# Performance work log

Hardware: AMD Instinct MI355X
Metric: run time of the kernel (lower is better)

The kernel has to match this reference:

```python
import jax, jax.numpy as jnp
import numpy as np

B, C, INTER, H, W = 4, 256, 128, 64, 64
EPS = 1e-5

def conv1x1(x, w, b):
    # x: [B,Cin,H,W], w: [Cout,Cin], b: [Cout]
    return jnp.einsum('bchw,oc->bohw', x, w) + b[None, :, None, None]

def setup_inputs() -> dict:
    key = jax.random.key(0)
    ks = jax.random.split(key, 12)
    sc_in = 1.0 / np.sqrt(C)
    sc_int = 1.0 / np.sqrt(INTER)
    return {
        'x': jax.random.normal(ks[0], (B, C, H, W), dtype=jnp.float32),
        'g_w': jax.random.normal(ks[1], (INTER, C), dtype=jnp.float32) * sc_in,
        'g_b': jax.random.normal(ks[2], (INTER,), dtype=jnp.float32) * 0.01,
        'theta_w': jax.random.normal(ks[3], (INTER, C), dtype=jnp.float32) * sc_in,
        'theta_b': jax.random.normal(ks[4], (INTER,), dtype=jnp.float32) * 0.01,
        'phi_w': jax.random.normal(ks[5], (INTER, C), dtype=jnp.float32) * sc_in,
        'phi_b': jax.random.normal(ks[6], (INTER,), dtype=jnp.float32) * 0.01,
        'w_w': jax.random.normal(ks[7], (C, INTER), dtype=jnp.float32) * sc_int,
        'w_b': jax.random.normal(ks[8], (C,), dtype=jnp.float32) * 0.01,
        'gamma': jax.random.normal(ks[9], (C,), dtype=jnp.float32) * 0.1 + 1.0,
        'beta': jax.random.normal(ks[10], (C,), dtype=jnp.float32) * 0.1,
    }

def reference(x, g_w, g_b, theta_w, theta_b, phi_w, phi_b, w_w, w_b, gamma, beta):
    b, c, h, w = x.shape
    n = h * w
    g_x = conv1x1(x, g_w, g_b).reshape(b, INTER, n).transpose(0, 2, 1)      # [b,n,d]
    theta_x = conv1x1(x, theta_w, theta_b).reshape(b, INTER, n).transpose(0, 2, 1)  # [b,n,d]
    phi_x = conv1x1(x, phi_w, phi_b).reshape(b, INTER, n)                   # [b,d,n]
    f = jnp.einsum('bnd,bdm->bnm', theta_x, phi_x)                          # [b,n,n]
    f_div_c = jax.nn.softmax(f, axis=-1)
    y = jnp.einsum('bnm,bmd->bnd', f_div_c, g_x)                            # [b,n,d]
    y = y.transpose(0, 2, 1).reshape(b, INTER, h, w)                        # [b,d,h,w]
    w_y = conv1x1(y, w_w, w_b)                                              # [b,c,h,w]
    # BatchNorm2d (training mode: batch statistics, biased variance)
    mean = jnp.mean(w_y, axis=(0, 2, 3), keepdims=True)
    var = jnp.var(w_y, axis=(0, 2, 3), keepdims=True)
    bn = (w_y - mean) * jax.lax.rsqrt(var + EPS)
    bn = bn * gamma[None, :, None, None] + beta[None, :, None, None]
    return bn + x
```

## Files before the change

### kernel.cpp

```cpp
#include <hip/hip_runtime.h>

#define B_ 4
#define C_ 256
#define D_ 128
#define N_ 4096
#define BN_ 16384

typedef unsigned short u16t;
typedef _Float16 f16t;
typedef f16t f16x8 __attribute__((ext_vector_type(8)));
typedef f16t f16x4 __attribute__((ext_vector_type(4)));
typedef float f32x4 __attribute__((ext_vector_type(4)));

static __device__ __forceinline__ u16t f2h(float f) {
  f16t h = (f16t)f; u16t u; __builtin_memcpy(&u, &h, 2); return u;
}
static __device__ __forceinline__ float h2f(u16t u) {
  f16t h; __builtin_memcpy(&h, &u, 2); return (float)h;
}

static __device__ __forceinline__ void gld_lds16(const u16t* g, u16t* l) {
  __builtin_amdgcn_global_load_lds(
      (const __attribute__((address_space(1))) void*)g,
      (__attribute__((address_space(3))) void*)l, 16, 0, 0);
}

__global__ __launch_bounds__(256) void prep_w(const float* __restrict__ th_w,
                                              const float* __restrict__ ph_w,
                                              const float* __restrict__ th_b,
                                              const float* __restrict__ ph_b,
                                              const float* __restrict__ g_w,
                                              const float* __restrict__ w_w,
                                              u16t* __restrict__ Wc, u16t* __restrict__ gwc,
                                              u16t* __restrict__ wwc, float* __restrict__ bc) {
  const int idx = blockIdx.x * 256 + threadIdx.x;
  if (idx < 65536) {
    const int j = idx >> 8, c = idx & 255;
    const float v = (j < 128) ? th_w[j * 256 + c] : ph_w[(j - 128) * 256 + c];
    Wc[idx] = f2h(v);
  } else if (idx < 98304) {
    const int i = idx - 65536;
    gwc[i] = f2h(g_w[i]);
  } else if (idx < 131072) {
    const int i = idx - 98304;
    wwc[i] = f2h(w_w[i]);
  } else if (idx < 131328) {
    const int j = idx - 131072;
    bc[j] = (j < 128) ? th_b[j] : ph_b[j - 128];
  }
}

__global__ __launch_bounds__(256) void transpose_x(const float* __restrict__ x,
                                                   u16t* __restrict__ xT) {
  __shared__ u16t t[32][33];
  const int b = blockIdx.z, c0 = blockIdx.y * 32, n0 = blockIdx.x * 32;
  const int tid = threadIdx.x;
  {
    const int cl = tid >> 3, n4 = (tid & 7) * 4;
    const float4 v = *(const float4*)(x + ((size_t)b * C_ + c0 + cl) * N_ + n0 + n4);
    t[n4 + 0][cl] = f2h(v.x);
    t[n4 + 1][cl] = f2h(v.y);
    t[n4 + 2][cl] = f2h(v.z);
    t[n4 + 3][cl] = f2h(v.w);
  }
  __syncthreads();
  {
    const int nl = tid >> 3, c4 = (tid & 7) * 4;
    unsigned int lo = (unsigned int)t[nl][c4 + 0] | ((unsigned int)t[nl][c4 + 1] << 16);
    unsigned int hi = (unsigned int)t[nl][c4 + 2] | ((unsigned int)t[nl][c4 + 3] << 16);
    uint2 o; o.x = lo; o.y = hi;
    *(uint2*)(xT + ((size_t)b * N_ + n0 + nl) * C_ + c0 + c4) = o;
  }
}

__global__ __launch_bounds__(256)
void gemm_qkv(const u16t* __restrict__ xT, const u16t* __restrict__ Wc,
              const u16t* __restrict__ gwc, const float* __restrict__ bc,
              const float* __restrict__ g_b, u16t* __restrict__ QKo,
              u16t* __restrict__ Vo) {
  __shared__ __attribute__((aligned(16))) u16t lA[128 * 40];
  __shared__ __attribute__((aligned(16))) u16t lB[128 * 40];
  const int z = blockIdx.z, bx = blockIdx.x;
  const u16t* xTb = xT + (size_t)z * N_ * C_;
  const u16t* A; const u16t* B; u16t* Cb; int ldc, m0, j0, colb;
  const float* bias;
  if (bx < 64) {
    A = xTb; B = Wc; Cb = QKo + (size_t)z * N_ * 256; ldc = 256;
    m0 = (bx >> 1) * 128; j0 = (bx & 1) * 128; bias = bc; colb = 1;
  } else {
    A = gwc; B = xTb; Cb = Vo + (size_t)z * D_ * N_; ldc = N_;
    m0 = 0; j0 = (bx - 64) * 128; bias = g_b; colb = 0;
  }
  const int tid = threadIdx.x, lane = tid & 63, wave = tid >> 6;
  const int quad = lane >> 4, l16 = lane & 15;
  const int wm = wave & 1, wj = wave >> 1;

  const f32x4 zero = {0.f, 0.f, 0.f, 0.f};
  f32x4 acc[4][4];
#pragma unroll
  for (int mi = 0; mi < 4; ++mi)
#pragma unroll
    for (int ji = 0; ji < 4; ++ji) acc[mi][ji] = zero;

  for (int k0 = 0; k0 < 256; k0 += 32) {
#pragma unroll
    for (int rr = 0; rr < 2; ++rr) {
      const int idx = rr * 256 + tid;
      const int row = idx >> 2, sg = idx & 3;
      *(uint4*)&lA[row * 40 + sg * 8] = *(const uint4*)(A + (size_t)(m0 + row) * 256 + k0 + sg * 8);
      *(uint4*)&lB[row * 40 + sg * 8] = *(const uint4*)(B + (size_t)(j0 + row) * 256 + k0 + sg * 8);
    }
    __syncthreads();
    f16x8 af[4], bfr[4];
#pragma unroll
    for (int i = 0; i < 4; ++i)
      af[i] = *(const f16x8*)&lA[(wm * 64 + i * 16 + l16) * 40 + quad * 8];
#pragma unroll
    for (int i = 0; i < 4; ++i)
      bfr[i] = *(const f16x8*)&lB[(wj * 64 + i * 16 + l16) * 40 + quad * 8];
#pragma unroll
    for (int mi = 0; mi < 4; ++mi)
#pragma unroll
      for (int ji = 0; ji < 4; ++ji)
        acc[mi][ji] = __builtin_amdgcn_mfma_f32_16x16x32_f16(af[mi], bfr[ji], acc[mi][ji], 0, 0, 0);
    __syncthreads();
  }

  float cb[4];
  if (colb) {
#pragma unroll
    for (int ji = 0; ji < 4; ++ji) cb[ji] = bias[j0 + wj * 64 + ji * 16 + l16];
  }
#pragma unroll
  for (int mi = 0; mi < 4; ++mi) {
#pragma unroll
    for (int r = 0; r < 4; ++r) {
      const int row = m0 + wm * 64 + mi * 16 + quad * 4 + r;
      const float rb = colb ? 0.f : bias[row];
#pragma unroll
      for (int ji = 0; ji < 4; ++ji) {
        const int col = j0 + wj * 64 + ji * 16 + l16;
        const float v = acc[mi][ji][r] + (colb ? cb[ji] : rb);
        Cb[(size_t)row * ldc + col] = f2h(v);
      }
    }
  }
}

__global__ __launch_bounds__(256, 2)
void attn(const u16t* __restrict__ QK, const u16t* __restrict__ V,
          u16t* __restrict__ On0, u16t* __restrict__ On1, float* __restrict__ ml) {
  const int b = blockIdx.y;
  const int split = blockIdx.z;
  const int n0 = blockIdx.x * 128;
  const int kv0 = split * (N_ / 4);
  const int tid = threadIdx.x, lane = tid & 63, wave = tid >> 6;
  const int quad = lane >> 4, l16 = lane & 15;
  const int x7 = l16 & 7;
  __shared__ __attribute__((aligned(16))) u16t Ks[2][64 * 128];
  __shared__ __attribute__((aligned(16))) u16t Vs[2][128 * 64];
  const u16t* QKb = QK + (size_t)b * N_ * 256;
  const u16t* Vb  = V  + (size_t)b * D_ * N_;

  const int krow_l = lane >> 4, kchunk_l = lane & 15;
  const int vrow_l = lane >> 3, vchunk_l = lane & 7;

  f16x8 qf[2][4];
#pragma unroll
  for (int qi = 0; qi < 2; ++qi) {
    const u16t* qrow = QKb + (size_t)(n0 + wave * 32 + qi * 16 + l16) * 256;
#pragma unroll
    for (int kc = 0; kc < 4; ++kc)
      qf[qi][kc] = *(const f16x8*)(qrow + kc * 32 + quad * 8);
  }

  const f32x4 zero = {0.f, 0.f, 0.f, 0.f};
  f32x4 o[2][8];
#pragma unroll
  for (int qi = 0; qi < 2; ++qi)
#pragma unroll
    for (int db = 0; db < 8; ++db) o[qi][db] = zero;
  float m[2] = {-1e30f, -1e30f}, l[2] = {0.f, 0.f};

#pragma unroll
  for (int i = 0; i < 4; ++i) {
    const int krow = (wave * 4 + i) * 4 + krow_l;
    const int kcl = kchunk_l ^ (krow & 7);
    gld_lds16(QKb + (size_t)(kv0 + krow) * 256 + 128 + kcl * 8,
              &Ks[0][(wave * 4 + i) * 512]);
  }
#pragma unroll
  for (int i = 0; i < 4; ++i) {
    const int vrow = (wave * 4 + i) * 8 + vrow_l;
    const int vcl = vchunk_l ^ (vrow & 7);
    gld_lds16(Vb + (size_t)vrow * N_ + kv0 + vcl * 8,
              &Vs[0][(wave * 4 + i) * 512]);
  }
  __syncthreads();

  int cur = 0;
  for (int it = 0; it < 16; ++it) {
    if (it < 15) {
      const int kvn = kv0 + (it + 1) * 64;
#pragma unroll
      for (int i = 0; i < 4; ++i) {
        const int krow = (wave * 4 + i) * 4 + krow_l;
        const int kcl = kchunk_l ^ (krow & 7);
        gld_lds16(QKb + (size_t)(kvn + krow) * 256 + 128 + kcl * 8,
                  &Ks[cur ^ 1][(wave * 4 + i) * 512]);
      }
#pragma unroll
      for (int i = 0; i < 4; ++i) {
        const int vrow = (wave * 4 + i) * 8 + vrow_l;
        const int vcl = vchunk_l ^ (vrow & 7);
        gld_lds16(Vb + (size_t)vrow * N_ + kvn + vcl * 8,
                  &Vs[cur ^ 1][(wave * 4 + i) * 512]);
      }
    }

    const u16t* KsC = &Ks[cur][0];
    const u16t* VsC = &Vs[cur][0];

    f32x4 s[2][4];
#pragma unroll
    for (int qi = 0; qi < 2; ++qi)
#pragma unroll
      for (int ci = 0; ci < 4; ++ci) s[qi][ci] = zero;
#pragma unroll
    for (int kc = 0; kc < 4; ++kc) {
#pragma unroll
      for (int ci = 0; ci < 4; ++ci) {
        f16x8 kf = *(const f16x8*)&KsC[(ci * 16 + l16) * 128 + (((kc * 4 + quad) ^ x7) << 3)];
        s[0][ci] = __builtin_amdgcn_mfma_f32_16x16x32_f16(kf, qf[0][kc], s[0][ci], 0, 0, 0);
        s[1][ci] = __builtin_amdgcn_mfma_f32_16x16x32_f16(kf, qf[1][kc], s[1][ci], 0, 0, 0);
      }
    }

    float al[2];
    f16x4 pb[2][4];
#pragma unroll
    for (int qi = 0; qi < 2; ++qi) {
      float mx = s[qi][0][0];
#pragma unroll
      for (int ci = 0; ci < 4; ++ci)
#pragma unroll
        for (int r = 0; r < 4; ++r) mx = fmaxf(mx, s[qi][ci][r]);
      mx = fmaxf(mx, __shfl_xor(mx, 16));
      mx = fmaxf(mx, __shfl_xor(mx, 32));
      const float mnew = fmaxf(m[qi], mx);
      al[qi] = __expf(m[qi] - mnew);
      float psum = 0.f;
#pragma unroll
      for (int ci = 0; ci < 4; ++ci) {
#pragma unroll
        for (int r = 0; r < 4; ++r) {
          const float p = __expf(s[qi][ci][r] - mnew);
          psum += p;
          pb[qi][ci][r] = (f16t)p;
        }
      }
      psum += __shfl_xor(psum, 16);
      psum += __shfl_xor(psum, 32);
      l[qi] = l[qi] * al[qi] + psum;
      m[qi] = mnew;
    }

#pragma unroll
    for (int qi = 0; qi < 2; ++qi)
#pragma unroll
      for (int db = 0; db < 8; ++db) {
#pragma unroll
        for (int r = 0; r < 4; ++r) o[qi][db][r] *= al[qi];
      }
#pragma unroll
    for (int ci = 0; ci < 4; ++ci) {
#pragma unroll
      for (int db = 0; db < 8; ++db) {
        f16x4 av = *(const f16x4*)&VsC[(db * 16 + l16) * 64 +
                                       (((ci * 2 + (quad >> 1)) ^ x7) << 3) + (quad & 1) * 4];
        o[0][db] = __builtin_amdgcn_mfma_f32_16x16x16f16(av, pb[0][ci], o[0][db], 0, 0, 0);
        o[1][db] = __builtin_amdgcn_mfma_f32_16x16x16f16(av, pb[1][ci], o[1][db], 0, 0, 0);
      }
    }
    __syncthreads();
    cur ^= 1;
  }

  u16t* Onb = (split < 2) ? On0 : On1;
  const int sp = split & 1;
#pragma unroll
  for (int qi = 0; qi < 2; ++qi) {
    const int q = n0 + wave * 32 + qi * 16 + l16;
    const float inv = 1.0f / l[qi];
    u16t* yrow = Onb + (((size_t)sp * B_ + b) * N_ + q) * D_;
#pragma unroll
    for (int db = 0; db < 8; ++db) {
      f16x4 pk;
#pragma unroll
      for (int r = 0; r < 4; ++r) pk[r] = (f16t)(o[qi][db][r] * inv);
      *(f16x4*)(yrow + db * 16 + quad * 4) = pk;
    }
    if (quad == 0) {
      float* mlp = ml + ((size_t)split * BN_ + (size_t)b * N_ + q) * 2;
      mlp[0] = m[qi]; mlp[1] = l[qi];
    }
  }
}

__global__ __launch_bounds__(256)
void gemm_wy(const u16t* __restrict__ wwc, const u16t* __restrict__ O0,
             const u16t* __restrict__ O2, const float* __restrict__ ml,
             u16t* __restrict__ wy, const float* __restrict__ w_b) {
  __shared__ __attribute__((aligned(16))) u16t lA[4][128 * 40];
  __shared__ __attribute__((aligned(16))) u16t lB[4][64 * 40];
  __shared__ float wrow[64][4];
  const int z = blockIdx.z;
  const int m0 = blockIdx.y * 128, j0 = blockIdx.x * 64;
  const int tid = threadIdx.x, lane = tid & 63, wave = tid >> 6;
  const int quad = lane >> 4, l16 = lane & 15;
  const int wm = wave & 1, wj = wave >> 1;
  const size_t halfO = (size_t)BN_ * D_;

  uint4 b0[4], b1[4], b2[4], b3[4];
#pragma unroll
  for (int cs = 0; cs < 4; ++cs) {
    const int cid = cs * 256 + tid;
    const int row = cid >> 4, sg = cid & 15;
    const size_t base = ((size_t)z * N_ + j0 + row) * D_ + sg * 8;
    b0[cs] = *(const uint4*)(O0 + base);
    b1[cs] = *(const uint4*)(O0 + halfO + base);
    b2[cs] = *(const uint4*)(O2 + base);
    b3[cs] = *(const uint4*)(O2 + halfO + base);
  }
  uint4 aw[8];
#pragma unroll
  for (int as = 0; as < 8; ++as) {
    const int cid = as * 256 + tid;
    const int row = cid >> 4, sg = cid & 15;
    aw[as] = *(const uint4*)(wwc + (size_t)(m0 + row) * 128 + sg * 8);
  }
  float mlv[8];
  if (tid < 64) {
    const int q = j0 + tid;
#pragma unroll
    for (int s = 0; s < 4; ++s) {
      mlv[2 * s]     = ml[((size_t)s * BN_ + (size_t)z * N_ + q) * 2];
      mlv[2 * s + 1] = ml[((size_t)s * BN_ + (size_t)z * N_ + q) * 2 + 1];
    }
  }

  if (tid < 64) {
    float mstar = -1e30f;
#pragma unroll
    for (int s = 0; s < 4; ++s) mstar = fmaxf(mstar, mlv[2 * s]);
    float w[4], wsum = 0.f;
#pragma unroll
    for (int s = 0; s < 4; ++s) { w[s] = __expf(mlv[2 * s] - mstar) * mlv[2 * s + 1]; wsum += w[s]; }
    const float inv = 1.0f / wsum;
#pragma unroll
    for (int s = 0; s < 4; ++s) wrow[tid][s] = w[s] * inv;
  }

#pragma unroll
  for (int as = 0; as < 8; ++as) {
    const int cid = as * 256 + tid;
    const int row = cid >> 4, sg = cid & 15;
    *(uint4*)&lA[sg >> 2][row * 40 + (sg & 3) * 8] = aw[as];
  }
  __syncthreads();

#pragma unroll
  for (int cs = 0; cs < 4; ++cs) {
    const int cid = cs * 256 + tid;
    const int row = cid >> 4, sg = cid & 15;
    const float w0 = wrow[row][0], w1 = wrow[row][1];
    const float w2 = wrow[row][2], w3 = wrow[row][3];
    const unsigned* p0 = &b0[cs].x; const unsigned* p1 = &b1[cs].x;
    const unsigned* p2 = &b2[cs].x; const unsigned* p3 = &b3[cs].x;
    uint4 y; unsigned* py = &y.x;
#pragma unroll
    for (int i = 0; i < 4; ++i) {
      const float lo = w0 * h2f((u16t)(p0[i] & 0xffff)) + w1 * h2f((u16t)(p1[i] & 0xffff)) +
                       w2 * h2f((u16t)(p2[i] & 0xffff)) + w3 * h2f((u16t)(p3[i] & 0xffff));
      const float hi = w0 * h2f((u16t)(p0[i] >> 16)) + w1 * h2f((u16t)(p1[i] >> 16)) +
                       w2 * h2f((u16t)(p2[i] >> 16)) + w3 * h2f((u16t)(p3[i] >> 16));
      py[i] = (unsigned)f2h(lo) | ((unsigned)f2h(hi) << 16);
    }
    *(uint4*)&lB[sg >> 2][row * 40 + (sg & 3) * 8] = y;
  }
  __syncthreads();

  const f32x4 zero = {0.f, 0.f, 0.f, 0.f};
  f32x4 acc[4][2];
#pragma unroll
  for (int mi = 0; mi < 4; ++mi)
#pragma unroll
    for (int ji = 0; ji < 2; ++ji) acc[mi][ji] = zero;
#pragma unroll
  for (int kc = 0; kc < 4; ++kc) {
    f16x8 af[4], bfr[2];
#pragma unroll
    for (int i = 0; i < 4; ++i)
      af[i] = *(const f16x8*)&lA[kc][(wm * 64 + i * 16 + l16) * 40 + quad * 8];
#pragma unroll
    for (int i = 0; i < 2; ++i)
      bfr[i] = *(const f16x8*)&lB[kc][(wj * 32 + i * 16 + l16) * 40 + quad * 8];
#pragma unroll
    for (int mi = 0; mi < 4; ++mi)
#pragma unroll
      for (int ji = 0; ji < 2; ++ji)
        acc[mi][ji] = __builtin_amdgcn_mfma_f32_16x16x32_f16(af[mi], bfr[ji], acc[mi][ji], 0, 0, 0);
  }

#pragma unroll
  for (int mi = 0; mi < 4; ++mi) {
#pragma unroll
    for (int r = 0; r < 4; ++r) {
      const int row = m0 + wm * 64 + mi * 16 + quad * 4 + r;
      const float rb = w_b[row];
#pragma unroll
      for (int ji = 0; ji < 2; ++ji) {
        const int col = j0 + wj * 32 + ji * 16 + l16;
        const float v = acc[mi][ji][r] + rb;
        wy[(size_t)z * C_ * N_ + (size_t)row * N_ + col] = f2h(v);
      }
    }
  }
}

__global__ __launch_bounds__(256) void bn_stats(const u16t* __restrict__ wy,
                                                float* __restrict__ stats) {
  const int c = blockIdx.x;
  const int tid = threadIdx.x, lane = tid & 63, wave = tid >> 6;
  __shared__ float red[8];
  float s1 = 0.f, s2 = 0.f;
#pragma unroll
  for (int it = 0; it < 8; ++it) {
    const int e = (it * 256 + tid) * 8;
    const int z = e >> 12, n = e & 4095;
    const uint4 v = *(const uint4*)(wy + (size_t)z * C_ * N_ + (size_t)c * N_ + n);
    const unsigned* p = &v.x;
#pragma unroll
    for (int i = 0; i < 4; ++i) {
      const float lo = h2f((u16t)(p[i] & 0xffff));
      const float hi = h2f((u16t)(p[i] >> 16));
      s1 += lo + hi;
      s2 += lo * lo + hi * hi;
    }
  }
  s1 += __shfl_xor(s1, 1);  s2 += __shfl_xor(s2, 1);
  s1 += __shfl_xor(s1, 2);  s2 += __shfl_xor(s2, 2);
  s1 += __shfl_xor(s1, 4);  s2 += __shfl_xor(s2, 4);
  s1 += __shfl_xor(s1, 8);  s2 += __shfl_xor(s2, 8);
  s1 += __shfl_xor(s1, 16); s2 += __shfl_xor(s2, 16);
  s1 += __shfl_xor(s1, 32); s2 += __shfl_xor(s2, 32);
  if (lane == 0) { red[wave] = s1; red[4 + wave] = s2; }
  __syncthreads();
  if (tid == 0) {
    stats[c]       = red[0] + red[1] + red[2] + red[3];
    stats[256 + c] = red[4] + red[5] + red[6] + red[7];
  }
}

__global__ __launch_bounds__(256) void bn_fin(const u16t* __restrict__ wy,
                                              const float* __restrict__ x,
                                              const float* __restrict__ stats,
                                              const float* __restrict__ gamma,
                                              const float* __restrict__ beta,
                                              float* __restrict__ out) {
  const int b = blockIdx.z, c = blockIdx.y;
  const int n4 = (blockIdx.x * 256 + threadIdx.x) * 4;
  const size_t off = ((size_t)b * C_ + c) * N_ + n4;
  const float inv_n = 1.0f / 16384.0f;
  const float mean = stats[c] * inv_n;
  const float var = stats[256 + c] * inv_n - mean * mean;
  const float rs = rsqrtf(var + 1e-5f);
  const float g = gamma[c], bt = beta[c];
  const uint2 wv = *(const uint2*)(wy + off);
  const float4 xv = *(const float4*)(x + off);
  float4 ov;
  ov.x = (h2f((u16t)(wv.x & 0xffff)) - mean) * rs * g + bt + xv.x;
  ov.y = (h2f((u16t)(wv.x >> 16))    - mean) * rs * g + bt + xv.y;
  ov.z = (h2f((u16t)(wv.y & 0xffff)) - mean) * rs * g + bt + xv.z;
  ov.w = (h2f((u16t)(wv.y >> 16))    - mean) * rs * g + bt + xv.w;
  *(float4*)(out + off) = ov;
}

extern "C" void kernel_launch(void* const* d_in, const int* in_sizes, int n_in,
                              void* d_out, int out_size, void* d_ws, size_t ws_size,
                              hipStream_t stream) {
  const float* x     = (const float*)d_in[0];
  const float* g_w   = (const float*)d_in[1];
  const float* g_b   = (const float*)d_in[2];
  const float* th_w  = (const float*)d_in[3];
  const float* th_b  = (const float*)d_in[4];
  const float* ph_w  = (const float*)d_in[5];
  const float* ph_b  = (const float*)d_in[6];
  const float* w_w   = (const float*)d_in[7];
  const float* w_b   = (const float*)d_in[8];
  const float* gamma = (const float*)d_in[9];
  const float* beta  = (const float*)d_in[10];
  float* out = (float*)d_out;
  char* ws = (char*)d_ws;

  u16t* O0  = (u16t*)(ws);
  u16t* QK  = (u16t*)(ws + 8388608);
  u16t* wy  = (u16t*)(ws + 8388608);
  u16t* V   = (u16t*)(ws + 16777216);
  u16t* Wc  = (u16t*)(ws + 20971520);
  u16t* gwc = (u16t*)(ws + 21102592);
  u16t* wwc = (u16t*)(ws + 21168128);
  float* bc = (float*)(ws + 21233664);
  float* stats = (float*)(ws + 21234688);
  float* ml = (float*)(ws + 21236736);
  u16t* O2 = (u16t*)d_out;

  prep_w<<<dim3(513), dim3(256), 0, stream>>>(th_w, ph_w, th_b, ph_b, g_w, w_w,
                                              Wc, gwc, wwc, bc);
  transpose_x<<<dim3(128, 8, B_), dim3(256), 0, stream>>>(x, (u16t*)ws);

  gemm_qkv<<<dim3(96, 1, B_), dim3(256), 0, stream>>>(
      (u16t*)ws, Wc, gwc, bc, g_b, QK, V);

  attn<<<dim3(32, B_, 4), dim3(256), 0, stream>>>(QK, V, O0, O2, ml);

  gemm_wy<<<dim3(64, 2, B_), dim3(256), 0, stream>>>(wwc, O0, O2, ml, wy, w_b);

  bn_stats<<<dim3(256), dim3(256), 0, stream>>>(wy, stats);

  bn_fin<<<dim3(4, 256, B_), dim3(256), 0, stream>>>(wy, x, stats, gamma, beta, out);
}
```

Baseline: 172.1 us.

## Defer softmax rescaling with threshold, tree-reduce max, and raise MFMA wave priority

Adds a lazy-rescale rule to the flash-attention loop: when the new tile max exceeds the running max by at most 8 for every lane in the wave, the running max is kept and the accumulator rescale is skipped. The row max is computed as a tree of fmaxf instead of a serial chain. s_setprio raises wave priority around the two MFMA blocks so matrix work gets scheduled ahead of other waves. The deferral relies on fp32 accumulators tolerating values up to e^8 above the stored max, and the fp16 P values can reach about 2981, which is within range.

```diff
diff --git a/kernel.cpp b/kernel.cpp
--- a/kernel.cpp
+++ b/kernel.cpp
@@ -226,6 +226,7 @@
     for (int qi = 0; qi < 2; ++qi)
 #pragma unroll
       for (int ci = 0; ci < 4; ++ci) s[qi][ci] = zero;
+    __builtin_amdgcn_s_setprio(1);
 #pragma unroll
     for (int kc = 0; kc < 4; ++kc) {
 #pragma unroll
@@ -235,20 +236,26 @@
         s[1][ci] = __builtin_amdgcn_mfma_f32_16x16x32_f16(kf, qf[1][kc], s[1][ci], 0, 0, 0);
       }
     }
-
+    __builtin_amdgcn_s_setprio(0);
+
+    f16x4 pb[2][4];
+    bool resc[2];
     float al[2];
-    f16x4 pb[2][4];
 #pragma unroll
     for (int qi = 0; qi < 2; ++qi) {
-      float mx = s[qi][0][0];
-#pragma unroll
-      for (int ci = 0; ci < 4; ++ci)
-#pragma unroll
-        for (int r = 0; r < 4; ++r) mx = fmaxf(mx, s[qi][ci][r]);
+      float m0_ = fmaxf(fmaxf(s[qi][0][0], s[qi][0][1]), fmaxf(s[qi][0][2], s[qi][0][3]));
+      float m1_ = fmaxf(fmaxf(s[qi][1][0], s[qi][1][1]), fmaxf(s[qi][1][2], s[qi][1][3]));
+      float m2_ = fmaxf(fmaxf(s[qi][2][0], s[qi][2][1]), fmaxf(s[qi][2][2], s[qi][2][3]));
+      float m3_ = fmaxf(fmaxf(s[qi][3][0], s[qi][3][1]), fmaxf(s[qi][3][2], s[qi][3][3]));
+      float mx = fmaxf(fmaxf(m0_, m1_), fmaxf(m2_, m3_));
       mx = fmaxf(mx, __shfl_xor(mx, 16));
       mx = fmaxf(mx, __shfl_xor(mx, 32));
-      const float mnew = fmaxf(m[qi], mx);
-      al[qi] = __expf(m[qi] - mnew);
+      const bool defer = __all(mx <= m[qi] + 8.f);
+      float mnew, alq;
+      if (defer) { mnew = m[qi]; alq = 1.f; } else {
+        mnew = fmaxf(m[qi], mx);
+        alq = __expf(m[qi] - mnew);
+      }
       float psum = 0.f;
 #pragma unroll
       for (int ci = 0; ci < 4; ++ci) {
@@ -261,17 +268,24 @@
       }
       psum += __shfl_xor(psum, 16);
       psum += __shfl_xor(psum, 32);
-      l[qi] = l[qi] * al[qi] + psum;
+      l[qi] = l[qi] * alq + psum;
       m[qi] = mnew;
-    }
-
-#pragma unroll
-    for (int qi = 0; qi < 2; ++qi)
-#pragma unroll
-      for (int db = 0; db < 8; ++db) {
-#pragma unroll
-        for (int r = 0; r < 4; ++r) o[qi][db][r] *= al[qi];
-      }
+      al[qi] = alq;
+      resc[qi] = !defer;
+    }
+
+#pragma unroll
+    for (int qi = 0; qi < 2; ++qi) {
+      if (resc[qi]) {
+#pragma unroll
+        for (int db = 0; db < 8; ++db) {
+#pragma unroll
+          for (int r = 0; r < 4; ++r) o[qi][db][r] *= al[qi];
+        }
+      }
+    }
+
+    __builtin_amdgcn_s_setprio(1);
 #pragma unroll
     for (int ci = 0; ci < 4; ++ci) {
 #pragma unroll
@@ -282,6 +296,7 @@
         o[1][db] = __builtin_amdgcn_mfma_f32_16x16x16f16(av, pb[1][ci], o[1][db], 0, 0, 0);
       }
     }
+    __builtin_amdgcn_s_setprio(0);
     __syncthreads();
     cur ^= 1;
   }
```

Result: slower. 176.6 us (+2.6%).
